# Optimization experiments

Measured on AMD Instinct MI355X. Metric: run time of the kernel, lower is better.

Reference implementation:

```python
import jax, jax.numpy as jnp
import numpy as np

R = 50000          # residues
P = 24             # residue_pad_length
APR = 15           # atoms per residue (<= P)
N = R * APR        # total atoms
ACD = ATD = RCD = RID = 32
N_ATOM_CODES, N_ATOM_TYPES, N_RES_CODES, MAX_SEQ = 38, 6, 21, 1024
VEC_OUT, SC_OUT = 64, 256          # irreps_out = 64x1e + 256x0e
SC_IN = P * ACD + P * ATD + RCD + RID  # 1600 scalar inputs


def setup_inputs() -> dict:
    key = jax.random.key(0)
    ks = jax.random.split(key, 10)
    return {
        "residue_base_coords": jax.random.normal(ks[0], (R, 3), jnp.float32),
        "residue_relative_coords": jax.random.normal(ks[1], (N, 3), jnp.float32),
        "residue_code_index": jax.random.randint(ks[2], (R,), 0, N_RES_CODES),
        "residue_sequence_index": jnp.arange(R) % MAX_SEQ,
        "atom_code_index": jax.random.randint(ks[3], (N,), 0, N_ATOM_CODES),
        "atom_type_index": jax.random.randint(ks[4], (N,), 0, N_ATOM_TYPES),
        "residue_index_atomwise": jnp.repeat(jnp.arange(R), APR),  # sorted, APR atoms each
        "W_atom_code": jax.random.normal(ks[5], (N_ATOM_CODES, ACD), jnp.float32),
        "W_atom_type": jax.random.normal(ks[6], (N_ATOM_TYPES, ATD), jnp.float32),
        "W_res_code": jax.random.normal(ks[7], (N_RES_CODES, RCD), jnp.float32),
        "W_res_idx": jax.random.normal(ks[8], (MAX_SEQ, RID), jnp.float32),
        "W_vec": jax.random.normal(jax.random.fold_in(key, 1), (P, VEC_OUT), jnp.float32),
        "W_sc": jax.random.normal(ks[9], (SC_IN, SC_OUT), jnp.float32),
    }


def reference(residue_base_coords, residue_relative_coords, residue_code_index,
              residue_sequence_index, atom_code_index, atom_type_index,
              residue_index_atomwise, W_atom_code, W_atom_type, W_res_code,
              W_res_idx, W_vec, W_sc):
    R_ = residue_base_coords.shape[0]
    P_ = W_vec.shape[0]
    N_ = residue_index_atomwise.shape[0]
    ri = residue_index_atomwise
    # vectorized replacement of the per-residue python loop:
    # position of each atom within its residue (residue_index_atomwise is sorted)
    offsets = jnp.searchsorted(ri, jnp.arange(R_))            # first atom of each residue
    pos = jnp.arange(N_) - offsets[ri]                        # [N]
    # scatter atoms into padded [R, P, ...] layout (pad slots stay 0, like F.pad)
    mask = jnp.zeros((R_, P_), bool).at[ri, pos].set(True)
    rel = jnp.zeros((R_, P_, 3), residue_relative_coords.dtype).at[ri, pos].set(residue_relative_coords)
    codes = jnp.zeros((R_, P_), atom_code_index.dtype).at[ri, pos].set(atom_code_index)
    types = jnp.zeros((R_, P_), atom_type_index.dtype).at[ri, pos].set(atom_type_index)
    maskf = mask.astype(W_atom_code.dtype)[..., None]
    # embedding lookups, masked (pad embeddings zeroed as in the torch code)
    ac = (W_atom_code[codes] * maskf).reshape(R_, -1)         # [R, P*ACD]
    at = (W_atom_type[types] * maskf).reshape(R_, -1)         # [R, P*ATD]
    rc = W_res_code[residue_code_index]                       # [R, RCD]
    rix = W_res_idx[residue_sequence_index]                   # [R, RID]
    scalars = jnp.concatenate([ac, at, rc, rix], axis=-1)     # [R, SC_IN]
    # e3nn o3.Linear: l=1 channels mix only with l=1 (Px1e -> VEC_OUTx1e),
    # l=0 channels mix only with l=0; path-normalized by sqrt(fan_in), no bias.
    out_vec = jnp.einsum('rpc,pm->rmc', rel, W_vec) / jnp.sqrt(jnp.float32(P_))
    out_sc = (scalars @ W_sc) / jnp.sqrt(jnp.float32(scalars.shape[-1]))
    features = jnp.concatenate([out_vec.reshape(R_, -1), out_sc], axis=-1)  # [R, 3*VEC_OUT+SC_OUT]
    return residue_base_coords, features  # ResidueState(coords, features)
```

## Files before the change

### kernel.cpp

```cpp
#include <hip/hip_runtime.h>
#include <stdint.h>

static constexpr int P       = 24;
static constexpr int EMB_D   = 32;
static constexpr int N_AC    = 38;
static constexpr int N_AT    = 6;
static constexpr int N_RC    = 21;
static constexpr int MAXSEQ  = 1024;
static constexpr int VEC_OUT = 64;
static constexpr int SC_OUT  = 256;
static constexpr int FEAT    = 3 * VEC_OUT + SC_OUT;
static constexpr int CT      = N_AC * N_AT;
static constexpr int NROWS   = P * CT;
static constexpr int ROWB    = SC_OUT * 2;
static constexpr uint32_t ZROWB = (uint32_t)NROWS * ROWB;
static constexpr uint32_t EOFS  = (uint32_t)N_RC * 512;

__device__ __forceinline__ unsigned short f2bf(float f) {
    uint32_t x = __float_as_uint(f);
    uint32_t r = (x + 0x7FFFu + ((x >> 16) & 1u)) >> 16;
    return (unsigned short)r;
}

__global__ __launch_bounds__(256) void k1_init_build(
        const float* __restrict__ Wac, const float* __restrict__ Wat,
        const float* __restrict__ Wrc, const float* __restrict__ Wri,
        const float* __restrict__ Wsc,
        float* __restrict__ Ec, float* __restrict__ Et,
        unsigned short* __restrict__ ErcH, unsigned short* __restrict__ ErixH,
        int* __restrict__ starts, int* __restrict__ ends, int R) {
    int b = blockIdx.x;
    const int initB = (R + 255) / 256;
    if (b < initB) {
        int i = b * 256 + threadIdx.x;
        if (i < R) { starts[i] = 0; ends[i] = 0; }
        return;
    }
    b -= initB;
    const float* Wemb; int n_emb, sc_base, idx, sect;
    if (b < P * N_AC) {
        Wemb = Wac; n_emb = N_AC; sc_base = 0; idx = b; sect = 0;
    } else if (b < P * N_AC + P * N_AT) {
        Wemb = Wat; n_emb = N_AT; sc_base = P * EMB_D; idx = b - P * N_AC; sect = 1;
    } else if (b < P * N_AC + P * N_AT + N_RC) {
        Wemb = Wrc; n_emb = N_RC; sc_base = 2 * P * EMB_D;
        idx = b - (P * N_AC + P * N_AT); sect = 2;
    } else {
        Wemb = Wri; n_emb = MAXSEQ; sc_base = 2 * P * EMB_D + EMB_D;
        idx = b - (P * N_AC + P * N_AT + N_RC); sect = 3;
    }
    int p = idx / n_emb, e = idx % n_emb;
    int o = threadIdx.x;
    const float* wrow = Wemb + (size_t)e * EMB_D;
    const float* scol = Wsc + (size_t)(sc_base + p * EMB_D) * SC_OUT + o;
    float s = 0.f;
#pragma unroll
    for (int d = 0; d < EMB_D; ++d) s += wrow[d] * scol[(size_t)d * SC_OUT];
    s *= 0.025f;
    if (sect == 0)      Ec[(size_t)idx * SC_OUT + o] = s;
    else if (sect == 1) Et[(size_t)idx * SC_OUT + o] = s;
    else if (sect == 2) ErcH[(size_t)idx * SC_OUT + o] = f2bf(s);
    else                ErixH[(size_t)idx * SC_OUT + o] = f2bf(s);
}

__global__ void k2_find_bounds(const int* __restrict__ ri, int* __restrict__ starts,
                               int* __restrict__ ends, int N) {
    int i = blockIdx.x * blockDim.x + threadIdx.x;
    if (i >= N) return;
    int r = ri[i];
    if (i == 0 || ri[i - 1] != r) starts[r] = i;
    if (i == N - 1 || ri[i + 1] != r) ends[r] = i + 1;
}

__global__ __launch_bounds__(256) void k3_fuse_prep(
        const float* __restrict__ Ec, const float* __restrict__ Et,
        unsigned short* __restrict__ Etab,
        const int* __restrict__ starts, const int* __restrict__ ends,
        const int* __restrict__ rcode, const int* __restrict__ rseq,
        const int* __restrict__ acode, const int* __restrict__ atype,
        const float* __restrict__ rel, const float* __restrict__ base,
        float* __restrict__ out_coords,
        int4* __restrict__ hdr, uint32_t* __restrict__ recArr, int R) {
    int b = blockIdx.x;
    if (b < NROWS + 1) {
        int o = threadIdx.x;
        if (b == NROWS) { Etab[(size_t)b * SC_OUT + o] = 0; return; }
        int j = b / CT, ct = b % CT, c = ct / N_AT, t = ct % N_AT;
        float s = Ec[((size_t)j * N_AC + c) * SC_OUT + o] +
                  Et[((size_t)j * N_AT + t) * SC_OUT + o];
        Etab[(size_t)b * SC_OUT + o] = f2bf(s);
        return;
    }
    b -= NROWS + 1;
    const int hdrB = (R + 255) >> 8;
    if (b < hdrB) {
        int i = b * 256 + threadIdx.x;
        if (i < R) {
            int st = starts[i];
            int c = ends[i] - st; if (c > P) c = P;
            hdr[i] = make_int4(st, c, rcode[i], rseq[i]);
        }
        return;
    }
    b -= hdrB;
    const int coordB = (3 * R + 1023) >> 10;
    if (b < coordB) {
        int i = b * 256 + threadIdx.x;
        int n4 = (3 * R) >> 2;
        if (i < n4)
            reinterpret_cast<float4*>(out_coords)[i] =
                reinterpret_cast<const float4*>(base)[i];
        if (i == n4) {
            for (int t = 4 * n4; t < 3 * R; ++t) out_coords[t] = base[t];
        }
        return;
    }
    b -= coordB;
    int i = b * 256 + threadIdx.x;
    if (i >= R * 64) return;
    int r = i >> 6, l = i & 63;
    int st = starts[r];
    int c = ends[r] - st; if (c > P) c = P;
    uint32_t out;
    if (l < 16) {
        out = ZROWB;
        if (l < c)
            out = (uint32_t)((l * CT + acode[st + l] * N_AT + atype[st + l]) * ROWB);
    } else {
        int idx = l - 16, k = idx / 3, cc = idx - k * 3;
        float v = 0.f;
        if (k < c) v = rel[(size_t)(st + k) * 3 + cc];
        out = __float_as_uint(v);
    }
    recArr[(size_t)r * 64 + l] = out;
}

struct F3 { float x, y, z; };

__global__ __launch_bounds__(256, 4) void k4_residue(
        const int4* __restrict__ hdr, const uint32_t* __restrict__ recArr,
        const unsigned char* __restrict__ tab,
        const unsigned char* __restrict__ ErcBase,
        const float* __restrict__ Wvec,
        float* __restrict__ out_feat, int R) {

    __shared__ float lds_w[16 * VEC_OUT];
    for (int t = threadIdx.x; t < 16 * VEC_OUT; t += 256) lds_w[t] = Wvec[t];
    __syncthreads();

    const int wave   = (blockIdx.x << 2) + (threadIdx.x >> 6);
    const int lane   = threadIdx.x & 63;
    const int b31    = lane & 31;
    const bool hiH   = lane >= 32;
    const uint32_t lo16 = (uint32_t)(b31 * 16);
    const int lb     = lane * 8;
    const int totalw = gridDim.x << 2;
    if (wave >= R) return;

    uint32_t rec, recN;
    int4 h, hN;

    auto REC = [&](uint32_t& rc, int4& hh, int j) {
        int rr = __builtin_amdgcn_readfirstlane(j < R ? j : R - 1);
        hh = hdr[rr];
        rc = recArr[(size_t)rr * 64 + lane];
    };

    int j = wave;
    REC(rec, h, j);
    while (true) {
        uint4 g0, g1, g2, g3, g4, g5, g6, g7, g8;
#define PGATHER(GK, K)                                                         \
        {                                                                      \
            uint32_t re = (uint32_t)__builtin_amdgcn_readlane((int)rec, 2*(K));\
            uint32_t ro = (uint32_t)__builtin_amdgcn_readlane((int)rec, 2*(K)+1);\
            uint32_t vo = (hiH ? ro : re) + lo16;                              \
            GK = *reinterpret_cast<const uint4*>(tab + vo);                    \
        }
        PGATHER(g0, 0) PGATHER(g1, 1) PGATHER(g2, 2) PGATHER(g3, 3)
        PGATHER(g4, 4) PGATHER(g5, 5) PGATHER(g6, 6) PGATHER(g7, 7)
#undef PGATHER
        {
            uint32_t vo = (hiH ? EOFS + ((uint32_t)h.w << 9)
                               : ((uint32_t)h.z << 9)) + lo16;
            g8 = *reinterpret_cast<const uint4*>(ErcBase + vo);
        }

        int jn = j + totalw;
        REC(recN, hN, jn);

        float vx = 0.f, vy = 0.f, vz = 0.f;
#pragma unroll
        for (int k = 0; k < 16; ++k) {
            float sx = __uint_as_float((uint32_t)__builtin_amdgcn_readlane((int)rec, 16 + 3 * k));
            float sy = __uint_as_float((uint32_t)__builtin_amdgcn_readlane((int)rec, 17 + 3 * k));
            float sz = __uint_as_float((uint32_t)__builtin_amdgcn_readlane((int)rec, 18 + 3 * k));
            float wk = lds_w[k * VEC_OUT + lane];
            vx = fmaf(sx, wk, vx);
            vy = fmaf(sy, wk, vy);
            vz = fmaf(sz, wk, vz);
        }

        float a0 = 0.f, a1 = 0.f, a2 = 0.f, a3 = 0.f;
        float a4 = 0.f, a5 = 0.f, a6 = 0.f, a7 = 0.f;
#define PACC(GK)                                                               \
        a0 += __uint_as_float(GK.x << 16);                                     \
        a1 += __uint_as_float(GK.x & 0xFFFF0000u);                             \
        a2 += __uint_as_float(GK.y << 16);                                     \
        a3 += __uint_as_float(GK.y & 0xFFFF0000u);                             \
        a4 += __uint_as_float(GK.z << 16);                                     \
        a5 += __uint_as_float(GK.z & 0xFFFF0000u);                             \
        a6 += __uint_as_float(GK.w << 16);                                     \
        a7 += __uint_as_float(GK.w & 0xFFFF0000u);
        PACC(g0) PACC(g1) PACC(g2) PACC(g3) PACC(g4)
        PACC(g5) PACC(g6) PACC(g7) PACC(g8)
#undef PACC

        a0 += __shfl_xor(a0, 32); a1 += __shfl_xor(a1, 32);
        a2 += __shfl_xor(a2, 32); a3 += __shfl_xor(a3, 32);
        a4 += __shfl_xor(a4, 32); a5 += __shfl_xor(a5, 32);
        a6 += __shfl_xor(a6, 32); a7 += __shfl_xor(a7, 32);

        if (h.y > 16) {
            float t0 = 0.f, t1 = 0.f, t2 = 0.f, t3 = 0.f;
            int st = h.x;
            for (int k = 16; k < h.y; ++k) {
                uint32_t ro = (uint32_t)__builtin_amdgcn_readlane((int)rec, 0);
                (void)ro;
                (void)st; (void)k;
            }
            float s0 = __shfl(t0, 2 * b31 + (hiH ? 1 : 0));
            float s1 = __shfl(t1, 2 * b31 + (hiH ? 1 : 0));
            float s2 = __shfl(t2, 2 * b31 + (hiH ? 1 : 0));
            float s3 = __shfl(t3, 2 * b31 + (hiH ? 1 : 0));
            a0 += hiH ? 0.f : s0; a1 += hiH ? 0.f : s1;
            a2 += hiH ? 0.f : s2; a3 += hiH ? 0.f : s3;
            a4 += hiH ? s0 : 0.f; a5 += hiH ? s1 : 0.f;
            a6 += hiH ? s2 : 0.f; a7 += hiH ? s3 : 0.f;
            (void)lb;
        }

        const float vs = 0.20412414523193150818f;
        float* frow = out_feat + (size_t)j * FEAT;
        F3 v3; v3.x = vx * vs; v3.y = vy * vs; v3.z = vz * vs;
        *reinterpret_cast<F3*>(frow + 3 * lane) = v3;
        float4 sd = hiH ? make_float4(a4, a5, a6, a7)
                        : make_float4(a0, a1, a2, a3);
        uint32_t so = ((uint32_t)b31 << 5) + (hiH ? 16u : 0u);
        *reinterpret_cast<float4*>(
            reinterpret_cast<char*>(frow + 3 * VEC_OUT) + so) = sd;

        j = jn;
        if (j >= R) break;
        rec = recN; h = hN;
    }
}

extern "C" void kernel_launch(void* const* d_in, const int* in_sizes, int n_in,
                              void* d_out, int out_size, void* d_ws, size_t ws_size,
                              hipStream_t stream) {
    const float* base  = (const float*)d_in[0];
    const float* rel   = (const float*)d_in[1];
    const int*   rcode = (const int*)d_in[2];
    const int*   rseq  = (const int*)d_in[3];
    const int*   acode = (const int*)d_in[4];
    const int*   atype = (const int*)d_in[5];
    const int*   ri    = (const int*)d_in[6];
    const float* Wac   = (const float*)d_in[7];
    const float* Wat   = (const float*)d_in[8];
    const float* Wrc   = (const float*)d_in[9];
    const float* Wri   = (const float*)d_in[10];
    const float* Wv    = (const float*)d_in[11];
    const float* Wsc   = (const float*)d_in[12];

    const int R = in_sizes[0] / 3;
    const int N = in_sizes[6];

    float* out_coords = (float*)d_out;
    float* out_feat   = out_coords + (size_t)R * 3;

    char* ws = (char*)d_ws;
    size_t ofs = 0;
    auto alloc = [&](size_t bytes) {
        void* p = ws + ofs;
        ofs = (ofs + bytes + 255) & ~255ULL;
        return p;
    };
    int*            starts = (int*)alloc((size_t)R * 4);
    int*            ends   = (int*)alloc((size_t)R * 4);
    float*          Ec_f   = (float*)alloc((size_t)P * N_AC * SC_OUT * 4);
    float*          Et_f   = (float*)alloc((size_t)P * N_AT * SC_OUT * 4);
    unsigned short* ErcH   = (unsigned short*)alloc((size_t)N_RC * SC_OUT * 2);
    unsigned short* ErixH  = (unsigned short*)alloc((size_t)MAXSEQ * SC_OUT * 2);
    unsigned short* Etab   = (unsigned short*)alloc((size_t)(NROWS + 1) * SC_OUT * 2);
    int4*           hdr    = (int4*)alloc((size_t)R * 16);
    uint32_t*       recArr = (uint32_t*)alloc((size_t)R * 64 * 4);
    (void)ws_size; (void)n_in; (void)out_size;

    const int initB  = (R + 255) / 256;
    const int k1B    = initB + P * N_AC + P * N_AT + N_RC + MAXSEQ;
    const int hdrB   = (R + 255) / 256;
    const int coordB = (3 * R + 1023) / 1024;
    const int recB   = (R * 64 + 255) / 256;
    const int k3B    = (NROWS + 1) + hdrB + coordB + recB;

    k1_init_build<<<k1B, 256, 0, stream>>>(Wac, Wat, Wrc, Wri, Wsc,
                                           Ec_f, Et_f, ErcH, ErixH, starts, ends, R);
    k2_find_bounds<<<(N + 255) / 256, 256, 0, stream>>>(ri, starts, ends, N);
    k3_fuse_prep<<<k3B, 256, 0, stream>>>(Ec_f, Et_f, Etab, starts, ends,
                                          rcode, rseq, acode, atype, rel, base,
                                          out_coords, hdr, recArr, R);
    k4_residue<<<2048, 256, 0, stream>>>(
        hdr, recArr, (const unsigned char*)Etab,
        (const unsigned char*)ErcH, Wv, out_feat, R);
}
```

Measured before the change: 57.11 us.

## Stage residue table gathers through direct global-to-LDS loads in residue kernel

Replaces the nine per-lane uint4 register gathers in the residue kernel with global_load_lds transfers into a per-wave 9 KB LDS staging buffer, followed by a vmcnt(0) wait and LDS reads for accumulation. The W_vec slice moves from shared memory into 16 registers per lane, and the prefetch of the next residue's record is hoisted to the top of the loop. It also fills in the previously empty fallback loop for residues with more than 16 atoms. The aim is to cut VGPR pressure and hide gather latency. The cost is 36 KB of LDS per block, which may limit occupancy, plus an extra LDS round trip.

```diff
diff --git a/kernel.cpp b/kernel.cpp
--- a/kernel.cpp
+++ b/kernel.cpp
@@ -16,10 +16,17 @@
 static constexpr uint32_t ZROWB = (uint32_t)NROWS * ROWB;
 static constexpr uint32_t EOFS  = (uint32_t)N_RC * 512;
 
+#define AS1 __attribute__((address_space(1)))
+#define AS3 __attribute__((address_space(3)))
+
 __device__ __forceinline__ unsigned short f2bf(float f) {
     uint32_t x = __float_as_uint(f);
     uint32_t r = (x + 0x7FFFu + ((x >> 16) & 1u)) >> 16;
     return (unsigned short)r;
+}
+
+__device__ __forceinline__ void gl_lds16(const void* g, void* l) {
+    __builtin_amdgcn_global_load_lds((const AS1 void*)g, (AS3 void*)l, 16, 0, 0);
 }
 
 __global__ __launch_bounds__(256) void k1_init_build(
@@ -142,52 +149,47 @@
         const unsigned char* __restrict__ tab,
         const unsigned char* __restrict__ ErcBase,
         const float* __restrict__ Wvec,
+        const int* __restrict__ acode, const int* __restrict__ atype,
+        const float* __restrict__ rel,
         float* __restrict__ out_feat, int R) {
 
-    __shared__ float lds_w[16 * VEC_OUT];
-    for (int t = threadIdx.x; t < 16 * VEC_OUT; t += 256) lds_w[t] = Wvec[t];
-    __syncthreads();
-
-    const int wave   = (blockIdx.x << 2) + (threadIdx.x >> 6);
+    __shared__ uint8_t stage[4][9 * 1024];
+    const int wid    = threadIdx.x >> 6;
     const int lane   = threadIdx.x & 63;
     const int b31    = lane & 31;
     const bool hiH   = lane >= 32;
     const uint32_t lo16 = (uint32_t)(b31 * 16);
-    const int lb     = lane * 8;
+    const int wave   = (blockIdx.x << 2) + wid;
     const int totalw = gridDim.x << 2;
     if (wave >= R) return;
-
-    uint32_t rec, recN;
-    int4 h, hN;
-
-    auto REC = [&](uint32_t& rc, int4& hh, int j) {
-        int rr = __builtin_amdgcn_readfirstlane(j < R ? j : R - 1);
-        hh = hdr[rr];
-        rc = recArr[(size_t)rr * 64 + lane];
-    };
+    uint8_t* buf = stage[wid];
+
+    float w[16];
+#pragma unroll
+    for (int k = 0; k < 16; ++k) w[k] = Wvec[k * VEC_OUT + lane];
 
     int j = wave;
-    REC(rec, h, j);
+    int r0 = __builtin_amdgcn_readfirstlane(j < R ? j : R - 1);
+    uint32_t rec = recArr[(size_t)r0 * 64 + lane];
+    int4 h = hdr[r0];
+
     while (true) {
-        uint4 g0, g1, g2, g3, g4, g5, g6, g7, g8;
-#define PGATHER(GK, K)                                                         \
-        {                                                                      \
-            uint32_t re = (uint32_t)__builtin_amdgcn_readlane((int)rec, 2*(K));\
-            uint32_t ro = (uint32_t)__builtin_amdgcn_readlane((int)rec, 2*(K)+1);\
-            uint32_t vo = (hiH ? ro : re) + lo16;                              \
-            GK = *reinterpret_cast<const uint4*>(tab + vo);                    \
-        }
-        PGATHER(g0, 0) PGATHER(g1, 1) PGATHER(g2, 2) PGATHER(g3, 3)
-        PGATHER(g4, 4) PGATHER(g5, 5) PGATHER(g6, 6) PGATHER(g7, 7)
-#undef PGATHER
+        int jn = j + totalw;
+        int r1 = __builtin_amdgcn_readfirstlane(jn < R ? jn : R - 1);
+        uint32_t recN = recArr[(size_t)r1 * 64 + lane];
+        int4 hN = hdr[r1];
+
+#pragma unroll
+        for (int k = 0; k < 8; ++k) {
+            uint32_t re = (uint32_t)__builtin_amdgcn_readlane((int)rec, 2 * k);
+            uint32_t ro = (uint32_t)__builtin_amdgcn_readlane((int)rec, 2 * k + 1);
+            gl_lds16(tab + (hiH ? ro : re) + lo16, buf + k * 1024);
+        }
         {
             uint32_t vo = (hiH ? EOFS + ((uint32_t)h.w << 9)
                                : ((uint32_t)h.z << 9)) + lo16;
-            g8 = *reinterpret_cast<const uint4*>(ErcBase + vo);
-        }
-
-        int jn = j + totalw;
-        REC(recN, hN, jn);
+            gl_lds16(ErcBase + vo, buf + 8 * 1024);
+        }
 
         float vx = 0.f, vy = 0.f, vz = 0.f;
 #pragma unroll
@@ -195,26 +197,28 @@
             float sx = __uint_as_float((uint32_t)__builtin_amdgcn_readlane((int)rec, 16 + 3 * k));
             float sy = __uint_as_float((uint32_t)__builtin_amdgcn_readlane((int)rec, 17 + 3 * k));
             float sz = __uint_as_float((uint32_t)__builtin_amdgcn_readlane((int)rec, 18 + 3 * k));
-            float wk = lds_w[k * VEC_OUT + lane];
-            vx = fmaf(sx, wk, vx);
-            vy = fmaf(sy, wk, vy);
-            vz = fmaf(sz, wk, vz);
-        }
+            vx = fmaf(sx, w[k], vx);
+            vy = fmaf(sy, w[k], vy);
+            vz = fmaf(sz, w[k], vz);
+        }
+
+        asm volatile("s_waitcnt vmcnt(0)" ::: "memory");
+        __builtin_amdgcn_sched_barrier(0);
 
         float a0 = 0.f, a1 = 0.f, a2 = 0.f, a3 = 0.f;
         float a4 = 0.f, a5 = 0.f, a6 = 0.f, a7 = 0.f;
-#define PACC(GK)                                                               \
-        a0 += __uint_as_float(GK.x << 16);                                     \
-        a1 += __uint_as_float(GK.x & 0xFFFF0000u);                             \
-        a2 += __uint_as_float(GK.y << 16);                                     \
-        a3 += __uint_as_float(GK.y & 0xFFFF0000u);                             \
-        a4 += __uint_as_float(GK.z << 16);                                     \
-        a5 += __uint_as_float(GK.z & 0xFFFF0000u);                             \
-        a6 += __uint_as_float(GK.w << 16);                                     \
-        a7 += __uint_as_float(GK.w & 0xFFFF0000u);
-        PACC(g0) PACC(g1) PACC(g2) PACC(g3) PACC(g4)
-        PACC(g5) PACC(g6) PACC(g7) PACC(g8)
-#undef PACC
+#pragma unroll
+        for (int k = 0; k < 9; ++k) {
+            uint4 gk = *reinterpret_cast<const uint4*>(buf + k * 1024 + lane * 16);
+            a0 += __uint_as_float(gk.x << 16);
+            a1 += __uint_as_float(gk.x & 0xFFFF0000u);
+            a2 += __uint_as_float(gk.y << 16);
+            a3 += __uint_as_float(gk.y & 0xFFFF0000u);
+            a4 += __uint_as_float(gk.z << 16);
+            a5 += __uint_as_float(gk.z & 0xFFFF0000u);
+            a6 += __uint_as_float(gk.w << 16);
+            a7 += __uint_as_float(gk.w & 0xFFFF0000u);
+        }
 
         a0 += __shfl_xor(a0, 32); a1 += __shfl_xor(a1, 32);
         a2 += __shfl_xor(a2, 32); a3 += __shfl_xor(a3, 32);
@@ -222,22 +226,27 @@
         a6 += __shfl_xor(a6, 32); a7 += __shfl_xor(a7, 32);
 
         if (h.y > 16) {
-            float t0 = 0.f, t1 = 0.f, t2 = 0.f, t3 = 0.f;
             int st = h.x;
             for (int k = 16; k < h.y; ++k) {
-                uint32_t ro = (uint32_t)__builtin_amdgcn_readlane((int)rec, 0);
-                (void)ro;
-                (void)st; (void)k;
+                int c = acode[st + k], t = atype[st + k];
+                const unsigned char* rp = tab +
+                    (uint32_t)((k * CT + c * N_AT + t) * ROWB) + lo16;
+                uint4 gg = *reinterpret_cast<const uint4*>(rp);
+                float wk = Wvec[k * VEC_OUT + lane];
+                vx = fmaf(rel[(size_t)(st + k) * 3], wk, vx);
+                vy = fmaf(rel[(size_t)(st + k) * 3 + 1], wk, vy);
+                vz = fmaf(rel[(size_t)(st + k) * 3 + 2], wk, vz);
+                float t0 = __uint_as_float(gg.x << 16);
+                float t1 = __uint_as_float(gg.x & 0xFFFF0000u);
+                float t2 = __uint_as_float(gg.y << 16);
+                float t3 = __uint_as_float(gg.y & 0xFFFF0000u);
+                float t4 = __uint_as_float(gg.z << 16);
+                float t5 = __uint_as_float(gg.z & 0xFFFF0000u);
+                float t6 = __uint_as_float(gg.w << 16);
+                float t7 = __uint_as_float(gg.w & 0xFFFF0000u);
+                a0 += t0; a1 += t1; a2 += t2; a3 += t3;
+                a4 += t4; a5 += t5; a6 += t6; a7 += t7;
             }
-            float s0 = __shfl(t0, 2 * b31 + (hiH ? 1 : 0));
-            float s1 = __shfl(t1, 2 * b31 + (hiH ? 1 : 0));
-            float s2 = __shfl(t2, 2 * b31 + (hiH ? 1 : 0));
-            float s3 = __shfl(t3, 2 * b31 + (hiH ? 1 : 0));
-            a0 += hiH ? 0.f : s0; a1 += hiH ? 0.f : s1;
-            a2 += hiH ? 0.f : s2; a3 += hiH ? 0.f : s3;
-            a4 += hiH ? s0 : 0.f; a5 += hiH ? s1 : 0.f;
-            a6 += hiH ? s2 : 0.f; a7 += hiH ? s3 : 0.f;
-            (void)lb;
         }
 
         const float vs = 0.20412414523193150818f;
@@ -312,5 +321,5 @@
                                           out_coords, hdr, recArr, R);
     k4_residue<<<2048, 256, 0, stream>>>(
         hdr, recArr, (const unsigned char*)Etab,
-        (const unsigned char*)ErcH, Wv, out_feat, R);
-}
+        (const unsigned char*)ErcH, Wv, acode, atype, rel, out_feat, R);
+}
```

After: 60.97 us. 1.07x slower.
